# Performance work log

Measured on AMD Instinct MI355X. Metric: run time of the kernel, lower is better.

Reference implementation:

```python
import jax, jax.numpy as jnp
import numpy as np

EPS = 1e-5
CONV_CFG = [(10, 5, 3), (8, 5, 2), (4, 2, 1), (3, 1, 1), (3, 1, 1)]  # (kernel, stride, pad)


def conv_bn_relu(x, w, gamma, beta, stride, pad):
    # x: [B, Cin, L], w: [Cout, Cin, K]; BatchNorm1d in training mode (batch stats)
    y = jax.lax.conv_general_dilated(x, w, (stride,), [(pad, pad)],
                                     dimension_numbers=('NCH', 'OIH', 'NCH'))
    mean = y.mean(axis=(0, 2), keepdims=True)
    var = y.var(axis=(0, 2), keepdims=True)
    y = (y - mean) * jax.lax.rsqrt(var + EPS)
    return jax.nn.relu(y * gamma[None, :, None] + beta[None, :, None])


def encoder(x, ws, bn_gamma, bn_beta):
    for i, (k, s, p) in enumerate(CONV_CFG):
        x = conv_bn_relu(x, ws[i], bn_gamma[i], bn_beta[i], s, p)
    return x


def gru(seq, h0, wih, whh, bih, bhh):
    # seq: [B, T, D], h0: [B, H]. torch GRU gate order: r, z, n.
    x_proj = jnp.einsum('btd,gd->btg', seq, wih) + bih  # [B, T, 3H]

    def step(h, xp):
        hp = h @ whh.T + bhh
        xr, xz, xn = jnp.split(xp, 3, axis=-1)
        hr, hz, hn = jnp.split(hp, 3, axis=-1)
        r = jax.nn.sigmoid(xr + hr)
        zg = jax.nn.sigmoid(xz + hz)
        n = jnp.tanh(xn + r * hn)
        h_new = (1.0 - zg) * n + zg * h
        return h_new, h_new

    h_last, outs = jax.lax.scan(step, h0, jnp.swapaxes(x_proj, 0, 1))
    return jnp.swapaxes(outs, 0, 1), h_last


def setup_inputs() -> dict:
    key = jax.random.key(0)
    ks = jax.random.split(key, 16)
    B, L, T = 64, 20480, 12
    x = jax.random.normal(ks[0], (B, 1, L), dtype=jnp.float32)
    hidden = jnp.zeros((1, B, 256), dtype=jnp.float32)
    shapes = [(512, 1, 10), (512, 512, 8), (512, 512, 4), (512, 512, 3), (512, 512, 3)]
    ws = {}
    for i, sh in enumerate(shapes):
        fan_out = sh[0] * sh[2]
        ws['w%d' % (i + 1)] = jax.random.normal(ks[1 + i], sh, dtype=jnp.float32) * np.float32(np.sqrt(2.0 / fan_out))
    bn_gamma = jnp.ones((5, 512), dtype=jnp.float32)
    bn_beta = jnp.zeros((5, 512), dtype=jnp.float32)
    gru_wih = jax.random.normal(ks[6], (768, 512), dtype=jnp.float32) * np.float32(np.sqrt(2.0 / 768.0))
    gru_whh = jax.random.normal(ks[7], (768, 256), dtype=jnp.float32) * np.float32(np.sqrt(2.0 / 768.0))
    gru_bih = jnp.zeros((768,), dtype=jnp.float32)
    gru_bhh = jnp.zeros((768,), dtype=jnp.float32)
    wk_w = jax.random.normal(ks[8], (T, 512, 256), dtype=jnp.float32) * np.float32(np.sqrt(2.0 / 512.0))
    wk_b = jnp.zeros((T, 512), dtype=jnp.float32)
    inp = dict(x=x, hidden=hidden, bn_gamma=bn_gamma, bn_beta=bn_beta,
               gru_wih=gru_wih, gru_whh=gru_whh, gru_bih=gru_bih, gru_bhh=gru_bhh,
               wk_w=wk_w, wk_b=wk_b, t_samples=200)
    inp.update(ws)
    return inp


def reference(x, hidden, w1, w2, w3, w4, w5, bn_gamma, bn_beta,
              gru_wih, gru_whh, gru_bih, gru_bhh, wk_w, wk_b, t_samples):
    B = x.shape[0]
    T = wk_w.shape[0]
    t = int(t_samples)
    z = encoder(x, (w1, w2, w3, w4, w5), bn_gamma, bn_beta)  # [B, 512, Lz]
    z = jnp.swapaxes(z, 1, 2)                                # [B, Lz, 512]
    encode_samples = jnp.swapaxes(z[:, t + 1:t + 1 + T, :], 0, 1)  # [T, B, 512]
    forward_seq = z[:, :t + 1, :]
    output, h_last = gru(forward_seq, hidden[0], gru_wih, gru_whh, gru_bih, gru_bhh)
    c_t = output[:, t, :]                                    # [B, 256]
    pred = jnp.einsum('bd,tkd->tbk', c_t, wk_w) + wk_b[:, None, :]  # [T, B, 512]
    total = jnp.einsum('tbk,tck->tbc', encode_samples, pred)        # [T, B, B]
    logsm = jax.nn.log_softmax(total, axis=-1)  # nn.LogSoftmax() on 2D -> dim=1
    nce = jnp.sum(jnp.diagonal(logsm, axis1=1, axis2=2)) / (-1.0 * B * T)
    # torch overwrites `correct` each iteration -> final value is from the last timestep
    correct = jnp.sum(jnp.argmax(jax.nn.softmax(total[-1], axis=-1), axis=0) == jnp.arange(B))
    accuracy = correct.astype(jnp.float32) / B
    return accuracy, nce, h_last[None]
```

## Files before the change

### kernel.cpp

```cpp
#include <hip/hip_runtime.h>
#include <hip/hip_bf16.h>

typedef __hip_bfloat16 bf16;
typedef short short8v __attribute__((ext_vector_type(8)));
typedef float float4v __attribute__((ext_vector_type(4)));

__device__ __forceinline__ float ld_f(const float* p, size_t i) { return p[i]; }
__device__ __forceinline__ float ld_f(const bf16* p, size_t i) { return __bfloat162float(p[i]); }
__device__ __forceinline__ float bfb_to_f(short u) {
    return __uint_as_float(((unsigned int)(unsigned short)u) << 16);
}
__device__ __forceinline__ short f_to_bf16bits(float v) {
    bf16 h = __float2bfloat16(v);
    short s; __builtin_memcpy(&s, &h, 2); return s;
}
__device__ __forceinline__ float sigmoidf_(float x) { return 1.0f / (1.0f + expf(-x)); }

__global__ __launch_bounds__(256) void zero_kernel(float* __restrict__ p, int n) {
    int i = blockIdx.x * 256 + threadIdx.x;
    if (i < n) p[i] = 0.0f;
}

__global__ __launch_bounds__(256) void pack_gemm(const float* __restrict__ w, short* __restrict__ out,
                                                 int M, int CIN, int KW, int KWP) {
    int idx = blockIdx.x * 256 + threadIdx.x;
    int tot = M * CIN * KWP;
    if (idx >= tot) return;
    int co = idx / (CIN * KWP);
    int r = idx - co * (CIN * KWP);
    int ci = r / KWP, t = r - ci * KWP;
    float v = (t < KW) ? w[((size_t)co * CIN + ci) * KW + t] : 0.0f;
    out[idx] = f_to_bf16bits(v);
}

__global__ __launch_bounds__(256) void pack_gruw(const float* __restrict__ whh, short* __restrict__ wfrag) {
    int idx = blockIdx.x * 256 + threadIdx.x;
    if (idx >= 196608) return;
    int j = idx & 7;
    int lane = (idx >> 3) & 63;
    int f = idx >> 9;
    int wv = f / 48;
    int r = f - wv * 48;
    int mt = r >> 3, kc = r & 7;
    int m = lane & 15, quad = lane >> 4;
    int row = (wv * 6 + mt) * 16 + m;
    int col = kc * 32 + quad * 8 + j;
    wfrag[idx] = f_to_bf16bits(whh[(size_t)row * 256 + col]);
}

template <int KWP, int ST, int SPANP>
__global__ __launch_bounds__(256, 3) void conv_mfma5(const bf16* __restrict__ in,
                                                     const short* __restrict__ wpk,
                                                     bf16* __restrict__ out,
                                                     int Lin, int Lout, int pad) {
    constexpr int KTOT = 512 * KWP;
    constexpr int NCHUNK = KTOT / 32;
    constexpr int CCC = 32 / KWP;
    constexpr int W16 = SPANP / 8;
    constexpr int NU = CCC * W16;
    constexpr int NLD = (NU + 255) / 256;

    const int l0 = blockIdx.x * 128;
    const int co0 = blockIdx.y * 128;
    const int tid = threadIdx.x;
    const int lane = tid & 63;
    const int wv = tid >> 6;
    const int m = lane & 15;
    const int quad = lane >> 4;
    const int nh = wv * 32;

    in += (size_t)blockIdx.z * 512 * Lin;
    out += (size_t)blockIdx.z * 512 * Lout;
    const short* ins = (const short*)in;

    __shared__ __align__(16) short As[2][128][40];
    __shared__ __align__(16) short rows[2][CCC][SPANP];

    const int base = ST * l0 - pad;
    const int g0a = base & ~7;
    const int off = base - g0a;

    const int arow = tid >> 2, aseg = tid & 3;

    float4v acc[8][2];
#pragma unroll
    for (int i = 0; i < 8; ++i) { acc[i][0] = (float4v){0,0,0,0}; acc[i][1] = (float4v){0,0,0,0}; }

    uint4 pa0, pa1;
    uint4 rbuf[NLD];

    auto load_stage = [&](int kc) {
        const int k0 = kc * 32;
        const int ci0 = kc * CCC;
        pa0 = *(const uint4*)(wpk + (size_t)(co0 + arow) * KTOT + k0 + aseg * 8);
        pa1 = *(const uint4*)(wpk + (size_t)(co0 + arow + 64) * KTOT + k0 + aseg * 8);
#pragma unroll
        for (int r = 0; r < NLD; ++r) {
            int e = tid + r * 256;
            if (NU % 256 == 0 || e < NU) {
                int cc = e / W16, col = e - cc * W16;
                int gs = g0a + col * 8;
                const short* src = ins + (size_t)(ci0 + cc) * Lin;
                if (gs >= 0 && gs + 8 <= Lin) {
                    rbuf[r] = *(const uint4*)(src + gs);
                } else {
                    ushort4 lo, hi;
#pragma unroll
                    for (int j = 0; j < 4; ++j) {
                        int g1 = gs + j, g2 = gs + 4 + j;
                        ((unsigned short*)&lo)[j] = (g1 >= 0 && g1 < Lin) ? (unsigned short)src[g1] : 0;
                        ((unsigned short*)&hi)[j] = (g2 >= 0 && g2 < Lin) ? (unsigned short)src[g2] : 0;
                    }
                    uint4 v;
                    v.x = lo.x | ((unsigned int)lo.y << 16);
                    v.y = lo.z | ((unsigned int)lo.w << 16);
                    v.z = hi.x | ((unsigned int)hi.y << 16);
                    v.w = hi.z | ((unsigned int)hi.w << 16);
                    rbuf[r] = v;
                }
            }
        }
    };
    auto commit = [&](int buf) {
        *(uint4*)&As[buf][arow][aseg * 8] = pa0;
        *(uint4*)&As[buf][arow + 64][aseg * 8] = pa1;
#pragma unroll
        for (int r = 0; r < NLD; ++r) {
            int e = tid + r * 256;
            if (NU % 256 == 0 || e < NU) {
                int cc = e / W16, col = e - cc * W16;
                *(uint4*)&rows[buf][cc][col * 8] = rbuf[r];
            }
        }
    };

    load_stage(0);
    commit(0);
    __syncthreads();

    for (int kc = 0; kc < NCHUNK; ++kc) {
        const int cur = kc & 1;
        if (kc + 1 < NCHUNK) load_stage(kc + 1);

        short8v afrag[8], bfrag[2];
#pragma unroll
        for (int s = 0; s < 8; ++s)
            afrag[s] = *(const short8v*)&As[cur][s * 16 + m][quad * 8];
#pragma unroll
        for (int t = 0; t < 2; ++t) {
            const int ll = nh + t * 16 + m;
            short8v bf;
            if constexpr (KWP == 8) {
                const short* rp = &rows[cur][quad][off + ST * ll];
#pragma unroll
                for (int j = 0; j < 8; ++j) bf[j] = rp[j];
            } else {
                const short* ra = &rows[cur][quad * 2 + 0][off + ST * ll];
                const short* rb = &rows[cur][quad * 2 + 1][off + ST * ll];
#pragma unroll
                for (int j = 0; j < 4; ++j) { bf[j] = ra[j]; bf[4 + j] = rb[j]; }
            }
            bfrag[t] = bf;
        }
#pragma unroll
        for (int s = 0; s < 8; ++s)
#pragma unroll
            for (int t = 0; t < 2; ++t)
                acc[s][t] = __builtin_amdgcn_mfma_f32_16x16x32_bf16(afrag[s], bfrag[t], acc[s][t], 0, 0, 0);

        if (kc + 1 < NCHUNK) commit(cur ^ 1);
        __syncthreads();
    }

#pragma unroll
    for (int t = 0; t < 2; ++t) {
        const int l = l0 + nh + t * 16 + m;
        if (l < Lout) {
#pragma unroll
            for (int s = 0; s < 8; ++s) {
#pragma unroll
                for (int reg = 0; reg < 4; ++reg) {
                    const int co = co0 + s * 16 + quad * 4 + reg;
                    out[(size_t)co * Lout + l] = __float2bfloat16(acc[s][t][reg]);
                }
            }
        }
    }
}

__global__ __launch_bounds__(256) void conv1_mfma(const float* __restrict__ x,
                                                  const short* __restrict__ w1p,
                                                  const float* __restrict__ ss,
                                                  bf16* __restrict__ y1c, int nbase) {
    const int l0 = blockIdx.x * 64;
    const int co0 = blockIdx.y * 128;
    const int nloc = blockIdx.z;
    const int n = nbase + nloc;
    const int tid = threadIdx.x;
    const int lane = tid & 63;
    const int wv = tid >> 6;
    const int m = lane & 15;
    const int quad = lane >> 4;

    __shared__ __align__(16) short xs[352];
    const int base = 5 * l0 - 3;
    for (int e = tid; e < 347; e += 256) {
        int g = base + e;
        float v = (g >= 0 && g < 20480) ? x[(size_t)n * 20480 + g] : 0.0f;
        xs[e] = f_to_bf16bits(v);
    }
    __syncthreads();

    const int lloc = wv * 16 + m;
    short8v bfrag;
    {
        const short* rp = &xs[5 * lloc + quad * 8];
#pragma unroll
        for (int j = 0; j < 8; ++j) bfrag[j] = rp[j];
    }
    float4v acc[8];
#pragma unroll
    for (int s = 0; s < 8; ++s) {
        short8v afrag = *(const short8v*)(w1p + (size_t)(co0 + s * 16 + m) * 32 + quad * 8);
        float4v z = (float4v){0.f, 0.f, 0.f, 0.f};
        acc[s] = __builtin_amdgcn_mfma_f32_16x16x32_bf16(afrag, bfrag, z, 0, 0, 0);
    }
    const int l = l0 + lloc;
#pragma unroll
    for (int s = 0; s < 8; ++s) {
#pragma unroll
        for (int reg = 0; reg < 4; ++reg) {
            const int co = co0 + s * 16 + quad * 4 + reg;
            float v = fmaxf(acc[s][reg] * ss[co] + ss[512 + co], 0.0f);
            y1c[((size_t)nloc * 512 + co) * 4096 + l] = __float2bfloat16(v);
        }
    }
}

__global__ __launch_bounds__(256) void conv1_stats(const float* __restrict__ x,
                                                   const float* __restrict__ w1,
                                                   float* __restrict__ sums) {
    const int n = blockIdx.x;
    const int tid = threadIdx.x;
    __shared__ __align__(16) float ws[5120];
    __shared__ __align__(16) float xs[5 * 256 + 10];
    for (int e = tid; e < 5120; e += 256) ws[e] = w1[e];
    const int co0 = tid, co1 = tid + 256;
    float a1_0 = 0.0f, a2_0 = 0.0f, a1_1 = 0.0f, a2_1 = 0.0f;
    for (int i = 0; i < 4; ++i) {
        const int c = blockIdx.y * 4 + i;
        const int base = c * 1280 - 3;
        __syncthreads();
        for (int e = tid; e < 1290; e += 256) {
            int g = base + e;
            xs[e] = (g >= 0 && g < 20480) ? x[(size_t)n * 20480 + g] : 0.0f;
        }
        __syncthreads();
        for (int l = 0; l < 256; ++l) {
            float y0 = 0.0f, y1v = 0.0f;
#pragma unroll
            for (int t = 0; t < 10; ++t) {
                float xv = xs[5 * l + t];
                y0 += ws[co0 * 10 + t] * xv;
                y1v += ws[co1 * 10 + t] * xv;
            }
            a1_0 += y0; a2_0 += y0 * y0;
            a1_1 += y1v; a2_1 += y1v * y1v;
        }
    }
    atomicAdd(&sums[co0], a1_0); atomicAdd(&sums[512 + co0], a2_0);
    atomicAdd(&sums[co1], a1_1); atomicAdd(&sums[512 + co1], a2_1);
}

__global__ __launch_bounds__(256) void bn1_finalize(const float* __restrict__ sums,
                                                    const float* __restrict__ gamma,
                                                    const float* __restrict__ beta,
                                                    float* __restrict__ ss) {
    int c = blockIdx.x * 256 + threadIdx.x;
    if (c >= 512) return;
    const float invM = 1.0f / (64.0f * 4096.0f);
    float mean = sums[c] * invM;
    float var = sums[512 + c] * invM - mean * mean;
    float sc = rsqrtf(var + 1e-5f) * gamma[c];
    ss[c] = sc;
    ss[512 + c] = beta[c] - mean * sc;
}

__global__ __launch_bounds__(256) void bn_stats_v(const bf16* __restrict__ y, float* __restrict__ sums, int L) {
    const int c = blockIdx.x, n = blockIdx.y;
    const short* p = (const short*)y + ((size_t)n * 512 + c) * L;
    float s1 = 0.f, s2 = 0.f;
    for (int l = threadIdx.x; l < L; l += 256) {
        float v = bfb_to_f(p[l]);
        s1 += v; s2 += v * v;
    }
#pragma unroll
    for (int off = 32; off > 0; off >>= 1) {
        s1 += __shfl_down(s1, off, 64);
        s2 += __shfl_down(s2, off, 64);
    }
    __shared__ float r1[4], r2[4];
    const int lane = threadIdx.x & 63, wv = threadIdx.x >> 6;
    if (lane == 0) { r1[wv] = s1; r2[wv] = s2; }
    __syncthreads();
    if (threadIdx.x == 0) {
        atomicAdd(&sums[c], r1[0] + r1[1] + r1[2] + r1[3]);
        atomicAdd(&sums[512 + c], r2[0] + r2[1] + r2[2] + r2[3]);
    }
}

__global__ __launch_bounds__(256) void bn_apply_v(bf16* __restrict__ y, const float* __restrict__ sums,
                                                  const float* __restrict__ gamma, const float* __restrict__ beta,
                                                  int layer, int L) {
    const int c = blockIdx.x, n = blockIdx.y;
    const float invM = 1.0f / (64.0f * (float)L);
    float mean = sums[c] * invM;
    float var = sums[512 + c] * invM - mean * mean;
    float sc = rsqrtf(var + 1e-5f) * gamma[layer * 512 + c];
    float sh = beta[layer * 512 + c] - mean * sc;
    short* p = (short*)y + ((size_t)n * 512 + c) * L;
    for (int l = threadIdx.x; l < L; l += 256) {
        float v = bfb_to_f(p[l]);
        p[l] = f_to_bf16bits(fmaxf(v * sc + sh, 0.0f));
    }
}

__global__ __launch_bounds__(256) void xproj_mfma(const bf16* __restrict__ y5,
                                                  const short* __restrict__ wihp,
                                                  const float* __restrict__ bih,
                                                  float* __restrict__ xp,
                                                  const int* __restrict__ tsamp) {
    const int t0 = blockIdx.x * 64;
    const int g0 = blockIdx.y * 128;
    const int b = blockIdx.z;
    const int tid = threadIdx.x;
    const int lane = tid & 63;
    const int wv = tid >> 6;
    const int m = lane & 15;
    const int quad = lane >> 4;
    const int ts = tsamp[0];

    __shared__ __align__(16) short As[128][40];
    __shared__ __align__(16) short Bt[32][66];

    float4v acc[8];
#pragma unroll
    for (int i = 0; i < 8; ++i) acc[i] = (float4v){0.f, 0.f, 0.f, 0.f};

    const short* y5s = (const short*)y5;
    for (int kc = 0; kc < 16; ++kc) {
        const int k0 = kc * 32;
        __syncthreads();
#pragma unroll
        for (int r = 0; r < 2; ++r) {
            int e = tid + r * 256;
            int row = e >> 2, seg = e & 3;
            *(uint4*)&As[row][seg * 8] =
                *(const uint4*)(wihp + (size_t)(g0 + row) * 512 + k0 + seg * 8);
        }
        for (int e = tid; e < 2048; e += 256) {
            int cc = e >> 6, tl = e & 63;
            Bt[cc][tl] = y5s[((size_t)b * 512 + k0 + cc) * 409 + t0 + tl];
        }
        __syncthreads();
        short8v bfrag;
#pragma unroll
        for (int j = 0; j < 8; ++j) bfrag[j] = Bt[quad * 8 + j][wv * 16 + m];
#pragma unroll
        for (int s = 0; s < 8; ++s) {
            short8v afrag = *(const short8v*)&As[s * 16 + m][quad * 8];
            acc[s] = __builtin_amdgcn_mfma_f32_16x16x32_bf16(afrag, bfrag, acc[s], 0, 0, 0);
        }
    }
    const int t = t0 + wv * 16 + m;
    if (t <= ts) {
#pragma unroll
        for (int s = 0; s < 8; ++s) {
#pragma unroll
            for (int reg = 0; reg < 4; ++reg) {
                const int g = g0 + s * 16 + quad * 4 + reg;
                xp[((size_t)b * 256 + t) * 768 + g] = acc[s][reg] + bih[g];
            }
        }
    }
}

__global__ __launch_bounds__(512, 2) void gru_mfma(const float* __restrict__ xproj,
                                                   const short* __restrict__ wfrag,
                                                   const float* __restrict__ hidden,
                                                   const float* __restrict__ bhh,
                                                   float* __restrict__ hlast,
                                                   const int* __restrict__ tsamp) {
    const int b = blockIdx.x;
    const int tid = threadIdx.x;
    const int lane = tid & 63;
    const int wv = tid >> 6;
    const int m = lane & 15;
    const int quad = lane >> 4;

    __shared__ float hf[256];
    __shared__ __align__(16) short hbs[256];
    __shared__ float pre[768];

    short8v wreg[48];
    {
        const short* wb = wfrag + ((size_t)(wv * 48) * 64 + lane) * 8;
#pragma unroll
        for (int f = 0; f < 48; ++f) wreg[f] = *(const short8v*)(wb + (size_t)f * 512);
    }
    if (wv < 4) {
        float hv = hidden[(size_t)b * 256 + tid];
        hf[tid] = hv;
        hbs[tid] = f_to_bf16bits(hv);
    }
    const int ts = tsamp[0];
    const float* xb = xproj + (size_t)b * 256 * 768;
    float bhr = 0.f, bhz = 0.f, bhn = 0.f, nxr = 0.f, nxz = 0.f, nxn = 0.f;
    if (wv < 4) {
        bhr = bhh[tid]; bhz = bhh[256 + tid]; bhn = bhh[512 + tid];
        nxr = xb[tid]; nxz = xb[256 + tid]; nxn = xb[512 + tid];
    }

    for (int step = 0; step <= ts; ++step) {
        __syncthreads();
        float4v acc[6];
#pragma unroll
        for (int i = 0; i < 6; ++i) acc[i] = (float4v){0.f, 0.f, 0.f, 0.f};
#pragma unroll
        for (int kc = 0; kc < 8; ++kc) {
            short8v bfrag = *(const short8v*)&hbs[kc * 32 + quad * 8];
#pragma unroll
            for (int mt = 0; mt < 6; ++mt)
                acc[mt] = __builtin_amdgcn_mfma_f32_16x16x32_bf16(wreg[mt * 8 + kc], bfrag, acc[mt], 0, 0, 0);
        }
        if (m == 0) {
#pragma unroll
            for (int mt = 0; mt < 6; ++mt)
#pragma unroll
                for (int reg = 0; reg < 4; ++reg)
                    pre[wv * 96 + mt * 16 + quad * 4 + reg] = acc[mt][reg];
        }
        __syncthreads();
        if (wv < 4) {
            const int g = tid;
            float r = sigmoidf_(nxr + bhr + pre[g]);
            float z = sigmoidf_(nxz + bhz + pre[256 + g]);
            float nn = tanhf(nxn + r * (bhn + pre[512 + g]));
            float hnew = (1.0f - z) * nn + z * hf[g];
            hf[g] = hnew;
            hbs[g] = f_to_bf16bits(hnew);
            if (step < ts) {
                const float* xs = xb + (size_t)(step + 1) * 768;
                nxr = xs[g]; nxz = xs[256 + g]; nxn = xs[512 + g];
            }
        }
    }
    __syncthreads();
    if (wv < 4) hlast[(size_t)b * 256 + tid] = hf[tid];
}

__global__ __launch_bounds__(256) void pred_kernel(const float* __restrict__ hlast, const float* __restrict__ wkw,
                                                   const float* __restrict__ wkb, float* __restrict__ pred) {
    const int c = blockIdx.x, t = blockIdx.y;
    __shared__ __align__(16) float hs[256];
    hs[threadIdx.x] = hlast[(size_t)c * 256 + threadIdx.x];
    __syncthreads();
    for (int k = threadIdx.x; k < 512; k += 256) {
        const float* wr = wkw + ((size_t)t * 512 + k) * 256;
        float acc = 0.0f;
        for (int d = 0; d < 256; d += 4) {
            float4 w4 = *(const float4*)&wr[d];
            acc += w4.x * hs[d] + w4.y * hs[d + 1] + w4.z * hs[d + 2] + w4.w * hs[d + 3];
        }
        pred[((size_t)t * 64 + c) * 512 + k] = acc + wkb[(size_t)t * 512 + k];
    }
}

__global__ __launch_bounds__(64) void total_kernel(const bf16* __restrict__ y5, const float* __restrict__ pred,
                                                   float* __restrict__ total, const int* __restrict__ tsamp) {
    const int b = blockIdx.x, t = blockIdx.y;
    const int col = tsamp[0] + 1 + t;
    __shared__ __align__(16) float es[512];
    for (int k = threadIdx.x; k < 512; k += 64) es[k] = ld_f(y5, ((size_t)b * 512 + k) * 409 + col);
    __syncthreads();
    const int c = threadIdx.x;
    const float* pr = pred + ((size_t)t * 64 + c) * 512;
    float acc = 0.0f;
    for (int k = 0; k < 512; k += 4) {
        float4 p4 = *(const float4*)&pr[k];
        acc += p4.x * es[k] + p4.y * es[k + 1] + p4.z * es[k + 2] + p4.w * es[k + 3];
    }
    total[((size_t)t * 64 + b) * 64 + c] = acc;
}

__global__ __launch_bounds__(256) void final_kernel(const float* __restrict__ total, const float* __restrict__ hlast,
                                                    float* __restrict__ out) {
    __shared__ float rowM[768], rowS[768];
    __shared__ float red[256];
    __shared__ int cnt[64];
    const int tid = threadIdx.x;
    float local = 0.0f;
    for (int row = tid; row < 768; row += 256) {
        const float* r = total + (size_t)row * 64;
        float m = r[0];
        for (int c = 1; c < 64; ++c) m = fmaxf(m, r[c]);
        float s = 0.0f;
        for (int c = 0; c < 64; ++c) s += expf(r[c] - m);
        rowM[row] = m; rowS[row] = s;
        int bcol = row & 63;
        local += r[bcol] - m - logf(s);
    }
    red[tid] = local;
    __syncthreads();
    for (int o = 128; o > 0; o >>= 1) {
        if (tid < o) red[tid] += red[tid + o];
        __syncthreads();
    }
    if (tid == 0) out[1] = red[0] / (-768.0f);
    if (tid < 64) {
        const int c = tid;
        float best = -1e30f; int bi = -1;
        for (int b = 0; b < 64; ++b) {
            int row = 11 * 64 + b;
            float v = expf(total[(size_t)row * 64 + c] - rowM[row]) / rowS[row];
            if (v > best) { best = v; bi = b; }
        }
        cnt[c] = (bi == c) ? 1 : 0;
    }
    __syncthreads();
    if (tid == 0) {
        int s = 0;
        for (int c = 0; c < 64; ++c) s += cnt[c];
        out[0] = (float)s / 64.0f;
    }
    for (int i = tid; i < 16384; i += 256) out[2 + i] = hlast[i];
}

extern "C" void kernel_launch(void* const* d_in, const int* in_sizes, int n_in,
                              void* d_out, int out_size, void* d_ws, size_t ws_size,
                              hipStream_t stream) {
    const float *x = nullptr, *hidden = nullptr, *gamma = nullptr, *beta = nullptr;
    const float *wih = nullptr, *whh = nullptr, *bih = nullptr, *bhh = nullptr;
    const float *wkw = nullptr, *wkb = nullptr;
    const float *w1 = nullptr, *w2 = nullptr, *w3 = nullptr, *w4 = nullptr, *w5 = nullptr;
    const int* tsamp = nullptr;
    for (int i = 0; i < n_in; ++i) {
        const float* p = (const float*)d_in[i];
        switch (in_sizes[i]) {
            case 1310720: x = p; break;
            case 16384:   hidden = p; break;
            case 2560:    if (!gamma) gamma = p; else beta = p; break;
            case 393216:  wih = p; break;
            case 196608:  whh = p; break;
            case 768:     if (!bih) bih = p; else bhh = p; break;
            case 1572864: wkw = p; break;
            case 6144:    wkb = p; break;
            case 1:       tsamp = (const int*)d_in[i]; break;
            case 5120:    w1 = p; break;
            case 2097152: w2 = p; break;
            case 1048576: w3 = p; break;
            case 786432:  if (!w4) w4 = p; else w5 = p; break;
            default: break;
        }
    }

    char* ws = (char*)d_ws;
    const size_t SLOT_B = 57872384ull;
    int NBC = 8;
    if (ws_size >= SLOT_B + 64ull * 4194304ull + 57344ull) NBC = 64;
    else if (ws_size >= SLOT_B + 32ull * 4194304ull + 57344ull) NBC = 32;
    else if (ws_size >= SLOT_B + 16ull * 4194304ull + 57344ull) NBC = 16;

    bf16*  y2    = (bf16*)(ws + 0);
    bf16*  y4    = (bf16*)(ws + 0);
    float* xp    = (float*)(ws + 0);
    short* wconv = (short*)(ws + 53676032ull);
    bf16*  y1c   = (bf16*)(ws + SLOT_B);
    bf16*  y3    = (bf16*)(ws + SLOT_B);
    bf16*  y5    = (bf16*)(ws + SLOT_B);
    const size_t tail = SLOT_B + (size_t)NBC * 4194304ull;
    float* sums  = (float*)(ws + tail);
    float* ss1   = (float*)(ws + tail + 20480ull);
    short* w1p   = (short*)(ws + tail + 24576ull);
    short* wihp  = (short*)(ws + 53676032ull);
    short* wfrag = (short*)(ws + 54462464ull);
    float* hlast = (float*)(ws + 54855680ull);
    float* pred  = (float*)(ws + 54921216ull);
    float* totl  = (float*)(ws + 56494080ull);

    zero_kernel<<<20, 256, 0, stream>>>(sums, 5120);
    conv1_stats<<<dim3(64, 4), 256, 0, stream>>>(x, w1, sums);
    bn1_finalize<<<2, 256, 0, stream>>>(sums, gamma, beta, ss1);
    pack_gemm<<<64, 256, 0, stream>>>(w1, w1p, 512, 1, 10, 32);

    pack_gemm<<<8192, 256, 0, stream>>>(w2, wconv, 512, 512, 8, 8);
    for (int nb = 0; nb < 64; nb += NBC) {
        conv1_mfma<<<dim3(64, 4, NBC), 256, 0, stream>>>(x, w1p, ss1, y1c, nb);
        conv_mfma5<8, 5, 656><<<dim3(7, 4, NBC), 256, 0, stream>>>(
            y1c, wconv, y2 + (size_t)nb * 512 * 819, 4096, 819, 2);
    }
    bn_stats_v<<<dim3(512, 64), 256, 0, stream>>>(y2, sums + 1024, 819);
    bn_apply_v<<<dim3(512, 64), 256, 0, stream>>>(y2, sums + 1024, gamma, beta, 1, 819);

    pack_gemm<<<4096, 256, 0, stream>>>(w3, wconv, 512, 512, 4, 4);
    conv_mfma5<4, 2, 272><<<dim3(4, 4, 64), 256, 0, stream>>>(y2, wconv, y3, 819, 409, 1);
    bn_stats_v<<<dim3(512, 64), 256, 0, stream>>>(y3, sums + 2048, 409);
    bn_apply_v<<<dim3(512, 64), 256, 0, stream>>>(y3, sums + 2048, gamma, beta, 2, 409);

    pack_gemm<<<4096, 256, 0, stream>>>(w4, wconv, 512, 512, 3, 4);
    conv_mfma5<4, 1, 144><<<dim3(4, 4, 64), 256, 0, stream>>>(y3, wconv, y4, 409, 409, 1);
    bn_stats_v<<<dim3(512, 64), 256, 0, stream>>>(y4, sums + 3072, 409);
    bn_apply_v<<<dim3(512, 64), 256, 0, stream>>>(y4, sums + 3072, gamma, beta, 3, 409);

    pack_gemm<<<4096, 256, 0, stream>>>(w5, wconv, 512, 512, 3, 4);
    conv_mfma5<4, 1, 144><<<dim3(4, 4, 64), 256, 0, stream>>>(y4, wconv, y5, 409, 409, 1);
    bn_stats_v<<<dim3(512, 64), 256, 0, stream>>>(y5, sums + 4096, 409);
    bn_apply_v<<<dim3(512, 64), 256, 0, stream>>>(y5, sums + 4096, gamma, beta, 4, 409);

    pack_gemm<<<1536, 256, 0, stream>>>(wih, wihp, 768, 512, 1, 1);
    pack_gruw<<<768, 256, 0, stream>>>(whh, wfrag);
    xproj_mfma<<<dim3(4, 6, 64), 256, 0, stream>>>(y5, wihp, bih, xp, tsamp);
    gru_mfma<<<64, 512, 0, stream>>>(xp, wfrag, hidden, bhh, hlast, tsamp);

    pred_kernel<<<dim3(64, 12), 256, 0, stream>>>(hlast, wkw, wkb, pred);
    total_kernel<<<dim3(64, 12), 64, 0, stream>>>(y5, pred, totl, tsamp);
    final_kernel<<<1, 256, 0, stream>>>(totl, hlast, (float*)d_out);
}
```

Measured before the change: 2.123 ms.

## Fuse BN stats into conv epilogue and BN apply into next conv's input load

When the workspace is large enough for a full batch, each conv layer now accumulates per-channel sum and sum-of-squares in its epilogue through shuffles, shared atomics and global atomics. This removes the separate bn_stats passes. The following conv applies the BN scale/shift and ReLU to input tiles while staging them into shared memory, which removes the bn_apply passes for layers 2-4. All weight packing for later layers is batched into one kernel into separate buffers. This trades several full-tensor read/write passes for extra ALU work and atomics in the conv kernels. Statistics are now computed from fp32 accumulators rather than the stored bf16 values, so results can differ slightly.

```diff
diff --git a/kernel.cpp b/kernel.cpp
--- a/kernel.cpp
+++ b/kernel.cpp
@@ -13,6 +13,14 @@
 __device__ __forceinline__ short f_to_bf16bits(float v) {
     bf16 h = __float2bfloat16(v);
     short s; __builtin_memcpy(&s, &h, 2); return s;
+}
+__device__ __forceinline__ unsigned int bn_pair(unsigned int u, float sc, float sh) {
+    float x0 = bfb_to_f((short)(u & 0xffffu));
+    float x1 = bfb_to_f((short)(u >> 16));
+    float y0 = fmaxf(fmaf(sc, x0, sh), 0.0f);
+    float y1 = fmaxf(fmaf(sc, x1, sh), 0.0f);
+    return (unsigned int)(unsigned short)f_to_bf16bits(y0) |
+           ((unsigned int)(unsigned short)f_to_bf16bits(y1) << 16);
 }
 __device__ __forceinline__ float sigmoidf_(float x) { return 1.0f / (1.0f + expf(-x)); }
 
@@ -48,11 +56,73 @@
     wfrag[idx] = f_to_bf16bits(whh[(size_t)row * 256 + col]);
 }
 
-template <int KWP, int ST, int SPANP>
-__global__ __launch_bounds__(256, 3) void conv_mfma5(const bf16* __restrict__ in,
+__global__ __launch_bounds__(256) void pack_all(const float* __restrict__ w3, const float* __restrict__ w4,
+                                                const float* __restrict__ w5, const float* __restrict__ wih,
+                                                const float* __restrict__ whh,
+                                                short* __restrict__ o3, short* __restrict__ o4,
+                                                short* __restrict__ o5, short* __restrict__ owih,
+                                                short* __restrict__ ogru) {
+    int idx = blockIdx.x * 256 + threadIdx.x;
+    const int NC = 512 * 512 * 4;
+    if (idx < NC) {
+        int co = idx >> 11, r = idx & 2047;
+        int ci = r >> 2, t = r & 3;
+        o3[idx] = f_to_bf16bits(w3[((size_t)co * 512 + ci) * 4 + t]);
+        return;
+    }
+    idx -= NC;
+    if (idx < NC) {
+        int co = idx >> 11, r = idx & 2047;
+        int ci = r >> 2, t = r & 3;
+        o4[idx] = (t < 3) ? f_to_bf16bits(w4[((size_t)co * 512 + ci) * 3 + t]) : 0;
+        return;
+    }
+    idx -= NC;
+    if (idx < NC) {
+        int co = idx >> 11, r = idx & 2047;
+        int ci = r >> 2, t = r & 3;
+        o5[idx] = (t < 3) ? f_to_bf16bits(w5[((size_t)co * 512 + ci) * 3 + t]) : 0;
+        return;
+    }
+    idx -= NC;
+    if (idx < 393216) {
+        owih[idx] = f_to_bf16bits(wih[idx]);
+        return;
+    }
+    idx -= 393216;
+    if (idx < 196608) {
+        int j = idx & 7;
+        int lane = (idx >> 3) & 63;
+        int f = idx >> 9;
+        int wv = f / 48;
+        int r = f - wv * 48;
+        int mt = r >> 3, kc = r & 7;
+        int m = lane & 15, quad = lane >> 4;
+        int row = (wv * 6 + mt) * 16 + m;
+        int col = kc * 32 + quad * 8 + j;
+        ogru[idx] = f_to_bf16bits(whh[(size_t)row * 256 + col]);
+    }
+}
+
+__global__ __launch_bounds__(256) void bn_fin(const float* __restrict__ sums, const float* __restrict__ gamma,
+                                              const float* __restrict__ beta, int layer, float invM,
+                                              float* __restrict__ ss) {
+    int c = blockIdx.x * 256 + threadIdx.x;
+    if (c >= 512) return;
+    float mean = sums[c] * invM;
+    float var = sums[512 + c] * invM - mean * mean;
+    float sc = rsqrtf(var + 1e-5f) * gamma[layer * 512 + c];
+    ss[c] = sc;
+    ss[512 + c] = beta[layer * 512 + c] - mean * sc;
+}
+
+template <int KWP, int ST, int SPANP, bool BNIN, bool STATS>
+__global__ __launch_bounds__(256, 3) void conv_mfma6(const bf16* __restrict__ in,
                                                      const short* __restrict__ wpk,
                                                      bf16* __restrict__ out,
-                                                     int Lin, int Lout, int pad) {
+                                                     int Lin, int Lout, int pad,
+                                                     const float* __restrict__ ssin,
+                                                     float* __restrict__ sums_out) {
     constexpr int KTOT = 512 * KWP;
     constexpr int NCHUNK = KTOT / 32;
     constexpr int CCC = 32 / KWP;
@@ -75,6 +145,7 @@
 
     __shared__ __align__(16) short As[2][128][40];
     __shared__ __align__(16) short rows[2][CCC][SPANP];
+    __shared__ float bsum[STATS ? 128 : 1][2];
 
     const int base = ST * l0 - pad;
     const int g0a = base & ~7;
@@ -104,38 +175,57 @@
                 if (gs >= 0 && gs + 8 <= Lin) {
                     rbuf[r] = *(const uint4*)(src + gs);
                 } else {
-                    ushort4 lo, hi;
-#pragma unroll
-                    for (int j = 0; j < 4; ++j) {
-                        int g1 = gs + j, g2 = gs + 4 + j;
-                        ((unsigned short*)&lo)[j] = (g1 >= 0 && g1 < Lin) ? (unsigned short)src[g1] : 0;
-                        ((unsigned short*)&hi)[j] = (g2 >= 0 && g2 < Lin) ? (unsigned short)src[g2] : 0;
+                    float sc = 0.f, sh = 0.f;
+                    if constexpr (BNIN) { sc = ssin[ci0 + cc]; sh = ssin[512 + ci0 + cc]; }
+                    unsigned short tmp[8];
+#pragma unroll
+                    for (int j = 0; j < 8; ++j) {
+                        int g = gs + j;
+                        float xv = 0.f;
+                        if (g >= 0 && g < Lin) {
+                            xv = bfb_to_f(src[g]);
+                            if constexpr (BNIN) xv = fmaxf(fmaf(sc, xv, sh), 0.0f);
+                        }
+                        tmp[j] = (unsigned short)f_to_bf16bits(xv);
                     }
                     uint4 v;
-                    v.x = lo.x | ((unsigned int)lo.y << 16);
-                    v.y = lo.z | ((unsigned int)lo.w << 16);
-                    v.z = hi.x | ((unsigned int)hi.y << 16);
-                    v.w = hi.z | ((unsigned int)hi.w << 16);
+                    v.x = tmp[0] | ((unsigned int)tmp[1] << 16);
+                    v.y = tmp[2] | ((unsigned int)tmp[3] << 16);
+                    v.z = tmp[4] | ((unsigned int)tmp[5] << 16);
+                    v.w = tmp[6] | ((unsigned int)tmp[7] << 16);
                     rbuf[r] = v;
                 }
             }
         }
     };
-    auto commit = [&](int buf) {
+    auto commit = [&](int buf, int kc) {
         *(uint4*)&As[buf][arow][aseg * 8] = pa0;
         *(uint4*)&As[buf][arow + 64][aseg * 8] = pa1;
+        const int ci0 = kc * CCC;
 #pragma unroll
         for (int r = 0; r < NLD; ++r) {
             int e = tid + r * 256;
             if (NU % 256 == 0 || e < NU) {
                 int cc = e / W16, col = e - cc * W16;
-                *(uint4*)&rows[buf][cc][col * 8] = rbuf[r];
+                uint4 v = rbuf[r];
+                if constexpr (BNIN) {
+                    int gs = g0a + col * 8;
+                    if (gs >= 0 && gs + 8 <= Lin) {
+                        float sc = ssin[ci0 + cc], sh = ssin[512 + ci0 + cc];
+                        v.x = bn_pair(v.x, sc, sh);
+                        v.y = bn_pair(v.y, sc, sh);
+                        v.z = bn_pair(v.z, sc, sh);
+                        v.w = bn_pair(v.w, sc, sh);
+                    }
+                }
+                *(uint4*)&rows[buf][cc][col * 8] = v;
             }
         }
     };
 
+    if (STATS && tid < 128) { bsum[tid][0] = 0.f; bsum[tid][1] = 0.f; }
     load_stage(0);
-    commit(0);
+    commit(0, 0);
     __syncthreads();
 
     for (int kc = 0; kc < NCHUNK; ++kc) {
@@ -168,14 +258,16 @@
             for (int t = 0; t < 2; ++t)
                 acc[s][t] = __builtin_amdgcn_mfma_f32_16x16x32_bf16(afrag[s], bfrag[t], acc[s][t], 0, 0, 0);
 
-        if (kc + 1 < NCHUNK) commit(cur ^ 1);
-        __syncthreads();
-    }
-
+        if (kc + 1 < NCHUNK) commit(cur ^ 1, kc + 1);
+        __syncthreads();
+    }
+
+    const bool v0 = (l0 + nh + m) < Lout;
+    const bool v1 = (l0 + nh + 16 + m) < Lout;
 #pragma unroll
     for (int t = 0; t < 2; ++t) {
         const int l = l0 + nh + t * 16 + m;
-        if (l < Lout) {
+        if (t ? v1 : v0) {
 #pragma unroll
             for (int s = 0; s < 8; ++s) {
 #pragma unroll
@@ -184,6 +276,40 @@
                     out[(size_t)co * Lout + l] = __float2bfloat16(acc[s][t][reg]);
                 }
             }
+        }
+    }
+
+    if constexpr (STATS) {
+#pragma unroll
+        for (int s = 0; s < 8; ++s) {
+            float p1[4], p2[4];
+#pragma unroll
+            for (int reg = 0; reg < 4; ++reg) {
+                float a0 = v0 ? acc[s][0][reg] : 0.f;
+                float a1 = v1 ? acc[s][1][reg] : 0.f;
+                p1[reg] = a0 + a1;
+                p2[reg] = a0 * a0 + a1 * a1;
+            }
+#pragma unroll
+            for (int o = 1; o <= 8; o <<= 1) {
+#pragma unroll
+                for (int reg = 0; reg < 4; ++reg) {
+                    p1[reg] += __shfl_xor(p1[reg], o);
+                    p2[reg] += __shfl_xor(p2[reg], o);
+                }
+            }
+            if (m == 0) {
+#pragma unroll
+                for (int reg = 0; reg < 4; ++reg) {
+                    atomicAdd(&bsum[s * 16 + quad * 4 + reg][0], p1[reg]);
+                    atomicAdd(&bsum[s * 16 + quad * 4 + reg][1], p2[reg]);
+                }
+            }
+        }
+        __syncthreads();
+        if (tid < 128) {
+            atomicAdd(&sums_out[co0 + tid], bsum[tid][0]);
+            atomicAdd(&sums_out[512 + co0 + tid], bsum[tid][1]);
         }
     }
 }
@@ -567,9 +693,9 @@
     char* ws = (char*)d_ws;
     const size_t SLOT_B = 57872384ull;
     int NBC = 8;
-    if (ws_size >= SLOT_B + 64ull * 4194304ull + 57344ull) NBC = 64;
-    else if (ws_size >= SLOT_B + 32ull * 4194304ull + 57344ull) NBC = 32;
-    else if (ws_size >= SLOT_B + 16ull * 4194304ull + 57344ull) NBC = 16;
+    if (ws_size >= SLOT_B + 64ull * 4194304ull + 81920ull) NBC = 64;
+    else if (ws_size >= SLOT_B + 32ull * 4194304ull + 81920ull) NBC = 32;
+    else if (ws_size >= SLOT_B + 16ull * 4194304ull + 81920ull) NBC = 16;
 
     bf16*  y2    = (bf16*)(ws + 0);
     bf16*  y4    = (bf16*)(ws + 0);
@@ -581,44 +707,83 @@
     const size_t tail = SLOT_B + (size_t)NBC * 4194304ull;
     float* sums  = (float*)(ws + tail);
     float* ss1   = (float*)(ws + tail + 20480ull);
-    short* w1p   = (short*)(ws + tail + 24576ull);
-    short* wihp  = (short*)(ws + 53676032ull);
-    short* wfrag = (short*)(ws + 54462464ull);
+    float* ss2   = (float*)(ws + tail + 24576ull);
+    float* ss3   = (float*)(ws + tail + 28672ull);
+    float* ss4   = (float*)(ws + tail + 32768ull);
+    short* w1p   = (short*)(ws + tail + 36864ull);
+
     float* hlast = (float*)(ws + 54855680ull);
     float* pred  = (float*)(ws + 54921216ull);
     float* totl  = (float*)(ws + 56494080ull);
+
+    short *wpk3, *wpk4, *wpk5, *wihp, *wfrag;
+    if (NBC == 64) {
+        wpk3  = (short*)(ws + SLOT_B + 33554432ull);
+        wpk4  = wpk3 + 1048576;
+        wpk5  = wpk4 + 1048576;
+        wihp  = wpk5 + 1048576;
+        wfrag = wihp + 393216;
+    } else {
+        wpk3 = wpk4 = wpk5 = wconv;
+        wihp  = (short*)(ws + 53676032ull);
+        wfrag = (short*)(ws + 54462464ull);
+    }
 
     zero_kernel<<<20, 256, 0, stream>>>(sums, 5120);
     conv1_stats<<<dim3(64, 4), 256, 0, stream>>>(x, w1, sums);
     bn1_finalize<<<2, 256, 0, stream>>>(sums, gamma, beta, ss1);
     pack_gemm<<<64, 256, 0, stream>>>(w1, w1p, 512, 1, 10, 32);
-
     pack_gemm<<<8192, 256, 0, stream>>>(w2, wconv, 512, 512, 8, 8);
-    for (int nb = 0; nb < 64; nb += NBC) {
-        conv1_mfma<<<dim3(64, 4, NBC), 256, 0, stream>>>(x, w1p, ss1, y1c, nb);
-        conv_mfma5<8, 5, 656><<<dim3(7, 4, NBC), 256, 0, stream>>>(
-            y1c, wconv, y2 + (size_t)nb * 512 * 819, 4096, 819, 2);
-    }
-    bn_stats_v<<<dim3(512, 64), 256, 0, stream>>>(y2, sums + 1024, 819);
-    bn_apply_v<<<dim3(512, 64), 256, 0, stream>>>(y2, sums + 1024, gamma, beta, 1, 819);
-
-    pack_gemm<<<4096, 256, 0, stream>>>(w3, wconv, 512, 512, 4, 4);
-    conv_mfma5<4, 2, 272><<<dim3(4, 4, 64), 256, 0, stream>>>(y2, wconv, y3, 819, 409, 1);
-    bn_stats_v<<<dim3(512, 64), 256, 0, stream>>>(y3, sums + 2048, 409);
-    bn_apply_v<<<dim3(512, 64), 256, 0, stream>>>(y3, sums + 2048, gamma, beta, 2, 409);
-
-    pack_gemm<<<4096, 256, 0, stream>>>(w4, wconv, 512, 512, 3, 4);
-    conv_mfma5<4, 1, 144><<<dim3(4, 4, 64), 256, 0, stream>>>(y3, wconv, y4, 409, 409, 1);
-    bn_stats_v<<<dim3(512, 64), 256, 0, stream>>>(y4, sums + 3072, 409);
-    bn_apply_v<<<dim3(512, 64), 256, 0, stream>>>(y4, sums + 3072, gamma, beta, 3, 409);
-
-    pack_gemm<<<4096, 256, 0, stream>>>(w5, wconv, 512, 512, 3, 4);
-    conv_mfma5<4, 1, 144><<<dim3(4, 4, 64), 256, 0, stream>>>(y4, wconv, y5, 409, 409, 1);
-    bn_stats_v<<<dim3(512, 64), 256, 0, stream>>>(y5, sums + 4096, 409);
-    bn_apply_v<<<dim3(512, 64), 256, 0, stream>>>(y5, sums + 4096, gamma, beta, 4, 409);
-
-    pack_gemm<<<1536, 256, 0, stream>>>(wih, wihp, 768, 512, 1, 1);
-    pack_gruw<<<768, 256, 0, stream>>>(whh, wfrag);
+
+    if (NBC == 64) {
+        conv1_mfma<<<dim3(64, 4, 64), 256, 0, stream>>>(x, w1p, ss1, y1c, 0);
+        conv_mfma6<8, 5, 656, false, true><<<dim3(7, 4, 64), 256, 0, stream>>>(
+            y1c, wconv, y2, 4096, 819, 2, nullptr, sums + 1024);
+        pack_all<<<14592, 256, 0, stream>>>(w3, w4, w5, wih, whh, wpk3, wpk4, wpk5, wihp, wfrag);
+        bn_fin<<<2, 256, 0, stream>>>(sums + 1024, gamma, beta, 1, 1.0f / (64.0f * 819.0f), ss2);
+
+        conv_mfma6<4, 2, 272, true, true><<<dim3(4, 4, 64), 256, 0, stream>>>(
+            y2, wpk3, y3, 819, 409, 1, ss2, sums + 2048);
+        bn_fin<<<2, 256, 0, stream>>>(sums + 2048, gamma, beta, 2, 1.0f / (64.0f * 409.0f), ss3);
+
+        conv_mfma6<4, 1, 144, true, true><<<dim3(4, 4, 64), 256, 0, stream>>>(
+            y3, wpk4, y4, 409, 409, 1, ss3, sums + 3072);
+        bn_fin<<<2, 256, 0, stream>>>(sums + 3072, gamma, beta, 3, 1.0f / (64.0f * 409.0f), ss4);
+
+        conv_mfma6<4, 1, 144, true, true><<<dim3(4, 4, 64), 256, 0, stream>>>(
+            y4, wpk5, y5, 409, 409, 1, ss4, sums + 4096);
+        bn_apply_v<<<dim3(512, 64), 256, 0, stream>>>(y5, sums + 4096, gamma, beta, 4, 409);
+    } else {
+        for (int nb = 0; nb < 64; nb += NBC) {
+            conv1_mfma<<<dim3(64, 4, NBC), 256, 0, stream>>>(x, w1p, ss1, y1c, nb);
+            conv_mfma6<8, 5, 656, false, false><<<dim3(7, 4, NBC), 256, 0, stream>>>(
+                y1c, wconv, y2 + (size_t)nb * 512 * 819, 4096, 819, 2, nullptr, nullptr);
+        }
+        bn_stats_v<<<dim3(512, 64), 256, 0, stream>>>(y2, sums + 1024, 819);
+        bn_apply_v<<<dim3(512, 64), 256, 0, stream>>>(y2, sums + 1024, gamma, beta, 1, 819);
+
+        pack_gemm<<<4096, 256, 0, stream>>>(w3, wconv, 512, 512, 4, 4);
+        conv_mfma6<4, 2, 272, false, false><<<dim3(4, 4, 64), 256, 0, stream>>>(
+            y2, wconv, y3, 819, 409, 1, nullptr, nullptr);
+        bn_stats_v<<<dim3(512, 64), 256, 0, stream>>>(y3, sums + 2048, 409);
+        bn_apply_v<<<dim3(512, 64), 256, 0, stream>>>(y3, sums + 2048, gamma, beta, 2, 409);
+
+        pack_gemm<<<4096, 256, 0, stream>>>(w4, wconv, 512, 512, 3, 4);
+        conv_mfma6<4, 1, 144, false, false><<<dim3(4, 4, 64), 256, 0, stream>>>(
+            y3, wconv, y4, 409, 409, 1, nullptr, nullptr);
+        bn_stats_v<<<dim3(512, 64), 256, 0, stream>>>(y4, sums + 3072, 409);
+        bn_apply_v<<<dim3(512, 64), 256, 0, stream>>>(y4, sums + 3072, gamma, beta, 3, 409);
+
+        pack_gemm<<<4096, 256, 0, stream>>>(w5, wconv, 512, 512, 3, 4);
+        conv_mfma6<4, 1, 144, false, false><<<dim3(4, 4, 64), 256, 0, stream>>>(
+            y4, wconv, y5, 409, 409, 1, nullptr, nullptr);
+        bn_stats_v<<<dim3(512, 64), 256, 0, stream>>>(y5, sums + 4096, 409);
+        bn_apply_v<<<dim3(512, 64), 256, 0, stream>>>(y5, sums + 4096, gamma, beta, 4, 409);
+
+        pack_gemm<<<1536, 256, 0, stream>>>(wih, wihp, 768, 512, 1, 1);
+        pack_gruw<<<768, 256, 0, stream>>>(whh, wfrag);
+    }
+
     xproj_mfma<<<dim3(4, 6, 64), 256, 0, stream>>>(y5, wihp, bih, xp, tsamp);
     gru_mfma<<<64, 512, 0, stream>>>(xp, wfrag, hidden, bhh, hlast, tsamp);
 
```

Result: no change. 2.120 ms (-0.1%).
